# Performance work log

Hardware: AMD Instinct MI355X
Metric: run time of the kernel (lower is better)

The kernel has to match this reference:

```python
import jax, jax.numpy as jnp
import numpy as np
from jax import lax

TF_ALPHA = 0.125


def _teacher_force(z, x, alpha):
    # z: (B, dz), x: (B, dx); force first dx dims of z where x is not NaN
    dx = x.shape[-1]
    head = z[:, :dx]
    forced = jnp.where(jnp.isnan(x), head, alpha * x + (1.0 - alpha) * head)
    return jnp.concatenate([forced, z[:, dx:]], axis=-1)


def setup_inputs() -> dict:
    key = jax.random.key(0)
    ks = jax.random.split(key, 8)
    B, T, dx, dz, dh, ds = 256, 1024, 64, 128, 512, 16
    X = jax.random.normal(ks[0], (B, T, dx), dtype=jnp.float32)
    inputs = jax.random.normal(ks[1], (B, T, ds), dtype=jnp.float32)
    # A in (0, 0.9) for stable linear part; small weight scales to avoid blowup over T steps
    A = jax.random.uniform(ks[2], (B, dz), dtype=jnp.float32) * 0.9
    W1 = jax.random.normal(ks[3], (B, dz, dh), dtype=jnp.float32) * (0.5 / np.sqrt(dh))
    W2 = jax.random.normal(ks[4], (B, dh, dz), dtype=jnp.float32) * (0.5 / np.sqrt(dz))
    h1 = jax.random.normal(ks[5], (B, dz), dtype=jnp.float32) * 0.1
    h2 = jax.random.normal(ks[6], (B, dh), dtype=jnp.float32) * 0.1
    C = jax.random.normal(ks[7], (B, dz, ds), dtype=jnp.float32) * (0.5 / np.sqrt(ds))
    return {"X": X, "inputs": inputs, "A": A, "W1": W1, "W2": W2,
            "h1": h1, "h2": h2, "C": C}


def _plrnn_forward(X, inputs, A, W1, W2, h1, h2, C):
    B, T, dx = X.shape
    dz = A.shape[-1]
    # z0 = zeros teacher-forced with alpha=1 from X[:, 0]
    z0 = jnp.zeros((B, dz), dtype=X.dtype)
    z0 = _teacher_force(z0, X[:, 0], alpha=1.0)

    Xt = jnp.transpose(X, (1, 0, 2))        # (T, B, dx)
    St = jnp.transpose(inputs, (1, 0, 2))   # (T, B, ds)

    def step(z, xs):
        x_t, s_t = xs
        zf = _teacher_force(z, x_t, TF_ALPHA)
        pre = jnp.einsum('bhz,bz->bh', W2, zf) + h2          # (B, dh)
        z_new = (A * zf
                 + jnp.einsum('bzh,bh->bz', W1, jax.nn.relu(pre))
                 + h1
                 + jnp.einsum('bzs,bs->bz', C, s_t))
        return z_new, z_new

    _, Z = lax.scan(step, z0, (Xt, St))      # Z: (T, B, dz)
    Z = jnp.transpose(Z, (1, 0, 2))          # (B, T, dz)
    return Z[:, :, :dx]                      # dim_x_proj == 0 path


def reference(X, inputs, A, W1, W2, h1, h2, C):
    return _plrnn_forward(X, inputs, A, W1, W2, h1, h2, C)
```

## Files before the change

kernel.cpp:

```cpp
#include <hip/hip_runtime.h>
#include <math.h>


#define NB 256
#define T  1024
#define DX 64
#define DZ 128
#define DH 512
#define DS 16

typedef _Float16 half8 __attribute__((ext_vector_type(8)));
typedef _Float16 v2h   __attribute__((ext_vector_type(2)));
typedef float    f32x4 __attribute__((ext_vector_type(4)));

__device__ __forceinline__ half8 cvt8(const float* __restrict__ src) {
  const float4 a = *reinterpret_cast<const float4*>(src);
  const float4 c = *reinterpret_cast<const float4*>(src + 4);
  half8 h;
  h[0] = (_Float16)a.x; h[1] = (_Float16)a.y; h[2] = (_Float16)a.z; h[3] = (_Float16)a.w;
  h[4] = (_Float16)c.x; h[5] = (_Float16)c.y; h[6] = (_Float16)c.z; h[7] = (_Float16)c.w;
  return h;
}

__global__ __launch_bounds__(512, 2) void plrnn_kernel(
    const float* __restrict__ X, const float* __restrict__ S,
    const float* __restrict__ A, const float* __restrict__ W1,
    const float* __restrict__ W2, const float* __restrict__ h1,
    const float* __restrict__ h2, const float* __restrict__ C,
    float* __restrict__ out)
{
  __shared__ _Float16 zf_h[DZ];
  __shared__ _Float16 r_h[8][64];
  __shared__ float    part[8][DZ];
  __shared__ float    s_lds[2][DS];

  const int b   = blockIdx.x;
  const int tid = threadIdx.x;
  const int w   = tid >> 6;
  const int l   = tid & 63;
  const int g   = l >> 4;
  const int r15 = l & 15;

  half8 w2f[4][4];
  #pragma unroll
  for (int mt = 0; mt < 4; ++mt)
    #pragma unroll
    for (int kt = 0; kt < 4; ++kt)
      w2f[mt][kt] = cvt8(W2 + ((size_t)b * DH + 64 * w + 16 * mt + r15) * DZ + 32 * kt + 8 * g);

  half8 w1f[8][2];
  #pragma unroll
  for (int mt = 0; mt < 8; ++mt)
    #pragma unroll
    for (int kt = 0; kt < 2; ++kt)
      w1f[mt][kt] = cvt8(W1 + ((size_t)b * DZ + 16 * mt + r15) * DH + 64 * w + 32 * kt + 8 * g);

  f32x4 h2v[4];
  #pragma unroll
  for (int mt = 0; mt < 4; ++mt)
    h2v[mt] = *reinterpret_cast<const f32x4*>(h2 + (size_t)b * DH + 64 * w + 16 * mt + 4 * g);

  float Areg = 0.f, h1reg = 0.f, zfreg = 0.f, xcur = 0.f, scur = 0.f;
  float Creg[DS];
  #pragma unroll
  for (int s = 0; s < DS; ++s) Creg[s] = 0.f;

  if (tid < DZ) {
    Areg  = A[(size_t)b * DZ + tid];
    h1reg = h1[(size_t)b * DZ + tid];
    #pragma unroll
    for (int s = 0; s < DS / 4; ++s) {
      const float4 v = *reinterpret_cast<const float4*>(C + ((size_t)b * DZ + tid) * DS + 4 * s);
      Creg[4*s+0] = v.x; Creg[4*s+1] = v.y; Creg[4*s+2] = v.z; Creg[4*s+3] = v.w;
    }
    float zfv = 0.f;
    if (tid < DX) {
      const float x = X[((size_t)b * T) * DX + tid];
      const float z0 = (x != x) ? 0.f : x;
      zfv = (x != x) ? z0 : (0.125f * x + 0.875f * z0);
      xcur = X[((size_t)b * T + 1) * DX + tid];
    }
    zf_h[tid] = (_Float16)zfv;
    zfreg = zfv;
  } else if (tid < DZ + DS) {
    s_lds[0][tid - DZ] = S[((size_t)b * T) * DS + (tid - DZ)];
    scur = S[((size_t)b * T + 1) * DS + (tid - DZ)];
  }
  __syncthreads();

  const f32x4 zero4 = {0.f, 0.f, 0.f, 0.f};

  for (int t = 0; t < T; ++t) {
    half8 bz[4];
    #pragma unroll
    for (int kt = 0; kt < 4; ++kt)
      bz[kt] = *reinterpret_cast<const half8*>(zf_h + 32 * kt + 8 * g);

    f32x4 acc1[4];
    #pragma unroll
    for (int mt = 0; mt < 4; ++mt) acc1[mt] = h2v[mt];
    #pragma unroll
    for (int kt = 0; kt < 4; ++kt)
      #pragma unroll
      for (int mt = 0; mt < 4; ++mt)
        acc1[mt] = __builtin_amdgcn_mfma_f32_16x16x32_f16(w2f[mt][kt], bz[kt], acc1[mt], 0, 0, 0);

    if (r15 == 0) {
      #pragma unroll
      for (int mt = 0; mt < 4; ++mt) {
        v2h p0, p1;
        p0.x = (_Float16)fmaxf(acc1[mt][0], 0.f);
        p0.y = (_Float16)fmaxf(acc1[mt][1], 0.f);
        p1.x = (_Float16)fmaxf(acc1[mt][2], 0.f);
        p1.y = (_Float16)fmaxf(acc1[mt][3], 0.f);
        *reinterpret_cast<v2h*>(&r_h[w][16 * mt + 4 * g])     = p0;
        *reinterpret_cast<v2h*>(&r_h[w][16 * mt + 4 * g + 2]) = p1;
      }
    }

    half8 br[2];
    #pragma unroll
    for (int kt = 0; kt < 2; ++kt)
      br[kt] = *reinterpret_cast<const half8*>(&r_h[w][32 * kt + 8 * g]);

    f32x4 acc2[8];
    #pragma unroll
    for (int mt = 0; mt < 8; ++mt) acc2[mt] = zero4;
    #pragma unroll
    for (int kt = 0; kt < 2; ++kt)
      #pragma unroll
      for (int mt = 0; mt < 8; ++mt)
        acc2[mt] = __builtin_amdgcn_mfma_f32_16x16x32_f16(w1f[mt][kt], br[kt], acc2[mt], 0, 0, 0);

    if (r15 == 0) {
      #pragma unroll
      for (int mt = 0; mt < 8; ++mt)
        *reinterpret_cast<f32x4*>(&part[w][16 * mt + 4 * g]) = acc2[mt];
    }
    __syncthreads();

    if (tid < DZ) {
      float u = 0.f;
      #pragma unroll
      for (int ww = 0; ww < 8; ++ww) u += part[ww][tid];
      float cs = 0.f;
      #pragma unroll
      for (int s = 0; s < DS; ++s) cs += Creg[s] * s_lds[t & 1][s];
      const float znew = Areg * zfreg + u + h1reg + cs;
      if (tid < DX) out[((size_t)b * T + t) * DX + tid] = znew;

      const float x = xcur;
      float zfv = znew;
      if (tid < DX) {
        zfv = (x != x) ? znew : (0.125f * x + 0.875f * znew);
        const int tn = (t + 2 < T) ? (t + 2) : (T - 1);
        xcur = X[((size_t)b * T + tn) * DX + tid];
      }
      zf_h[tid] = (_Float16)zfv;
      zfreg = zfv;
    } else if (tid < DZ + DS) {
      s_lds[(t + 1) & 1][tid - DZ] = scur;
      const int tn = (t + 2 < T) ? (t + 2) : (T - 1);
      scur = S[((size_t)b * T + tn) * DS + (tid - DZ)];
    }
    __syncthreads();
  }
}

extern "C" void kernel_launch(void* const* d_in, const int* in_sizes, int n_in,
                              void* d_out, int out_size, void* d_ws, size_t ws_size,
                              hipStream_t stream) {
  const float* X  = (const float*)d_in[0];
  const float* S  = (const float*)d_in[1];
  const float* A  = (const float*)d_in[2];
  const float* W1 = (const float*)d_in[3];
  const float* W2 = (const float*)d_in[4];
  const float* h1 = (const float*)d_in[5];
  const float* h2 = (const float*)d_in[6];
  const float* C  = (const float*)d_in[7];
  float* out = (float*)d_out;
  plrnn_kernel<<<dim3(NB), dim3(512), 0, stream>>>(X, S, A, W1, W2, h1, h2, C, out);
}
```

Measured before the change: 1.267 ms.

## Stage X, S and output in LDS chunks instead of per-step global accesses

Preloads 128-step chunks of the X and S inputs into shared memory with wide vectorized loads. Per-step outputs are buffered in shared memory and written back to global memory once per chunk. This replaces the scalar global load and store on every serial timestep, so global latency leaves the recurrence critical path. LDS use grows by about 72KB per block, which may limit occupancy under the 2-blocks launch bound, and each chunk boundary adds a bulk transfer plus an extra barrier. It also merges the relu result stores into single 4-wide half stores.

```diff
diff --git a/kernel.cpp b/kernel.cpp
--- a/kernel.cpp
+++ b/kernel.cpp
@@ -8,9 +8,10 @@
 #define DZ 128
 #define DH 512
 #define DS 16
+#define CHUNK 128
 
 typedef _Float16 half8 __attribute__((ext_vector_type(8)));
-typedef _Float16 v2h   __attribute__((ext_vector_type(2)));
+typedef _Float16 v4h   __attribute__((ext_vector_type(4)));
 typedef float    f32x4 __attribute__((ext_vector_type(4)));
 
 __device__ __forceinline__ half8 cvt8(const float* __restrict__ src) {
@@ -29,10 +30,12 @@
     const float* __restrict__ h2, const float* __restrict__ C,
     float* __restrict__ out)
 {
-  __shared__ _Float16 zf_h[DZ];
-  __shared__ _Float16 r_h[8][64];
-  __shared__ float    part[8][DZ];
-  __shared__ float    s_lds[2][DS];
+  __shared__ __align__(16) _Float16 zf_h[DZ];
+  __shared__ __align__(16) _Float16 r_h[8][64];
+  __shared__ __align__(16) float    part[8][DZ];
+  __shared__ __align__(16) float    Xc[CHUNK][DX];
+  __shared__ __align__(16) float    Sc[CHUNK][DS];
+  __shared__ __align__(16) float    outc[CHUNK][DX];
 
   const int b   = blockIdx.x;
   const int tid = threadIdx.x;
@@ -41,6 +44,20 @@
   const int g   = l >> 4;
   const int r15 = l & 15;
 
+  {
+    #pragma unroll
+    for (int k = 0; k < 4; ++k) {
+      const int flat = k * 2048 + tid * 4;
+      int srow = 1 + (flat >> 6);
+      if (srow > T - 1) srow = T - 1;
+      const float4 v = *reinterpret_cast<const float4*>(X + ((size_t)b * T + srow) * DX + (flat & 63));
+      *reinterpret_cast<float4*>(&((float*)Xc)[flat]) = v;
+    }
+    const int flat = tid * 4;
+    const float4 v = *reinterpret_cast<const float4*>(S + ((size_t)b * T) * DS + flat);
+    *reinterpret_cast<float4*>(&((float*)Sc)[flat]) = v;
+  }
+
   half8 w2f[4][4];
   #pragma unroll
   for (int mt = 0; mt < 4; ++mt)
@@ -60,7 +77,7 @@
   for (int mt = 0; mt < 4; ++mt)
     h2v[mt] = *reinterpret_cast<const f32x4*>(h2 + (size_t)b * DH + 64 * w + 16 * mt + 4 * g);
 
-  float Areg = 0.f, h1reg = 0.f, zfreg = 0.f, xcur = 0.f, scur = 0.f;
+  float Areg = 0.f, h1reg = 0.f, zfreg = 0.f;
   float Creg[DS];
   #pragma unroll
   for (int s = 0; s < DS; ++s) Creg[s] = 0.f;
@@ -78,19 +95,38 @@
       const float x = X[((size_t)b * T) * DX + tid];
       const float z0 = (x != x) ? 0.f : x;
       zfv = (x != x) ? z0 : (0.125f * x + 0.875f * z0);
-      xcur = X[((size_t)b * T + 1) * DX + tid];
     }
     zf_h[tid] = (_Float16)zfv;
     zfreg = zfv;
-  } else if (tid < DZ + DS) {
-    s_lds[0][tid - DZ] = S[((size_t)b * T) * DS + (tid - DZ)];
-    scur = S[((size_t)b * T + 1) * DS + (tid - DZ)];
   }
   __syncthreads();
 
   const f32x4 zero4 = {0.f, 0.f, 0.f, 0.f};
 
   for (int t = 0; t < T; ++t) {
+    if ((t & (CHUNK - 1)) == 0 && t) {
+      const int c0 = t - CHUNK;
+      #pragma unroll
+      for (int k = 0; k < 4; ++k) {
+        const int flat = k * 2048 + tid * 4;
+        const float4 v = *reinterpret_cast<const float4*>(&((float*)outc)[flat]);
+        *reinterpret_cast<float4*>(out + ((size_t)b * T + c0) * DX + flat) = v;
+      }
+      #pragma unroll
+      for (int k = 0; k < 4; ++k) {
+        const int flat = k * 2048 + tid * 4;
+        int srow = t + 1 + (flat >> 6);
+        if (srow > T - 1) srow = T - 1;
+        const float4 v = *reinterpret_cast<const float4*>(X + ((size_t)b * T + srow) * DX + (flat & 63));
+        *reinterpret_cast<float4*>(&((float*)Xc)[flat]) = v;
+      }
+      const int flat = tid * 4;
+      const float4 v = *reinterpret_cast<const float4*>(S + ((size_t)b * T + t) * DS + flat);
+      *reinterpret_cast<float4*>(&((float*)Sc)[flat]) = v;
+      __syncthreads();
+    }
+    const int tc = t & (CHUNK - 1);
+
     half8 bz[4];
     #pragma unroll
     for (int kt = 0; kt < 4; ++kt)
@@ -108,13 +144,12 @@
     if (r15 == 0) {
       #pragma unroll
       for (int mt = 0; mt < 4; ++mt) {
-        v2h p0, p1;
-        p0.x = (_Float16)fmaxf(acc1[mt][0], 0.f);
-        p0.y = (_Float16)fmaxf(acc1[mt][1], 0.f);
-        p1.x = (_Float16)fmaxf(acc1[mt][2], 0.f);
-        p1.y = (_Float16)fmaxf(acc1[mt][3], 0.f);
-        *reinterpret_cast<v2h*>(&r_h[w][16 * mt + 4 * g])     = p0;
-        *reinterpret_cast<v2h*>(&r_h[w][16 * mt + 4 * g + 2]) = p1;
+        v4h p;
+        p.x = (_Float16)fmaxf(acc1[mt][0], 0.f);
+        p.y = (_Float16)fmaxf(acc1[mt][1], 0.f);
+        p.z = (_Float16)fmaxf(acc1[mt][2], 0.f);
+        p.w = (_Float16)fmaxf(acc1[mt][3], 0.f);
+        *reinterpret_cast<v4h*>(&r_h[w][16 * mt + 4 * g]) = p;
       }
     }
 
@@ -145,25 +180,33 @@
       for (int ww = 0; ww < 8; ++ww) u += part[ww][tid];
       float cs = 0.f;
       #pragma unroll
-      for (int s = 0; s < DS; ++s) cs += Creg[s] * s_lds[t & 1][s];
+      for (int s = 0; s < DS / 4; ++s) {
+        const float4 sv = *reinterpret_cast<const float4*>(&Sc[tc][4 * s]);
+        cs += Creg[4*s+0] * sv.x + Creg[4*s+1] * sv.y
+            + Creg[4*s+2] * sv.z + Creg[4*s+3] * sv.w;
+      }
       const float znew = Areg * zfreg + u + h1reg + cs;
-      if (tid < DX) out[((size_t)b * T + t) * DX + tid] = znew;
-
-      const float x = xcur;
+
       float zfv = znew;
       if (tid < DX) {
+        outc[tc][tid] = znew;
+        const float x = Xc[tc][tid];
         zfv = (x != x) ? znew : (0.125f * x + 0.875f * znew);
-        const int tn = (t + 2 < T) ? (t + 2) : (T - 1);
-        xcur = X[((size_t)b * T + tn) * DX + tid];
       }
       zf_h[tid] = (_Float16)zfv;
       zfreg = zfv;
-    } else if (tid < DZ + DS) {
-      s_lds[(t + 1) & 1][tid - DZ] = scur;
-      const int tn = (t + 2 < T) ? (t + 2) : (T - 1);
-      scur = S[((size_t)b * T + tn) * DS + (tid - DZ)];
     }
     __syncthreads();
+  }
+
+  {
+    const int c0 = T - CHUNK;
+    #pragma unroll
+    for (int k = 0; k < 4; ++k) {
+      const int flat = k * 2048 + tid * 4;
+      const float4 v = *reinterpret_cast<const float4*>(&((float*)outc)[flat]);
+      *reinterpret_cast<float4*>(out + ((size_t)b * T + c0) * DX + flat) = v;
+    }
   }
 }
 
```

Measured after the change: 1.197 ms. -5.5%, faster.
